# Kernel tuning notes

Hardware: AMD Instinct MI355X
Metric: run time of the kernel (lower is better)

Reference implementation:

```python
import jax, jax.numpy as jnp
import numpy as np

N = 100000
E = 1600000
IN_C = 256
HID = 128
OUT_C = 128
HEADS = 4
C_HEAD = HID // HEADS
BN_EPS = 1e-5
NEG_SLOPE = 0.2


def setup_inputs() -> dict:
    key = jax.random.key(0)
    ks = jax.random.split(key, 12)
    s = lambda fan: 1.0 / np.sqrt(fan)
    return {
        "x": jax.random.normal(ks[0], (N, IN_C), dtype=jnp.float32),
        "W_gat": jax.random.normal(ks[1], (IN_C, HID), dtype=jnp.float32) * s(IN_C),
        "att_src": jax.random.normal(ks[2], (HEADS, C_HEAD), dtype=jnp.float32) * s(C_HEAD),
        "att_dst": jax.random.normal(ks[3], (HEADS, C_HEAD), dtype=jnp.float32) * s(C_HEAD),
        "bias_gat": jnp.zeros((HID,), dtype=jnp.float32),
        "bn1_gamma": jnp.ones((HID,), dtype=jnp.float32),
        "bn1_beta": jnp.zeros((HID,), dtype=jnp.float32),
        "eps_gin": jnp.zeros((), dtype=jnp.float32),
        "lin_W": jax.random.normal(ks[4], (HID, OUT_C), dtype=jnp.float32) * s(HID),
        "lin_b": jnp.zeros((OUT_C,), dtype=jnp.float32),
        "bn2_gamma": jnp.ones((OUT_C,), dtype=jnp.float32),
        "bn2_beta": jnp.zeros((OUT_C,), dtype=jnp.float32),
        "edge_index": jax.random.randint(ks[5], (2, E), 0, N, dtype=jnp.int64),
    }


def batch_norm(h, gamma, beta):
    mu = jnp.mean(h, axis=0)
    var = jnp.var(h, axis=0)
    return (h - mu) * jax.lax.rsqrt(var + BN_EPS) * gamma + beta


def reference(x, W_gat, att_src, att_dst, bias_gat, bn1_gamma, bn1_beta,
              eps_gin, lin_W, lin_b, bn2_gamma, bn2_beta, edge_index):
    src, dst = edge_index[0], edge_index[1]
    # ---- GATConv ----
    h = (x @ W_gat).reshape(N, HEADS, C_HEAD)              # [N,H,C]
    a_src = jnp.einsum('nhc,hc->nh', h, att_src)            # [N,H]
    a_dst = jnp.einsum('nhc,hc->nh', h, att_dst)            # [N,H]
    e = jax.nn.leaky_relu(a_src[src] + a_dst[dst], NEG_SLOPE)  # [E,H]
    # segment softmax over incoming edges of each dst node
    m = jax.ops.segment_max(e, dst, num_segments=N)         # [N,H]
    num = jnp.exp(e - m[dst])                                # [E,H]
    den = jax.ops.segment_sum(num, dst, num_segments=N)      # [N,H]
    alpha = num / den[dst]                                   # [E,H]
    msg = alpha[:, :, None] * h[src]                         # [E,H,C]
    out1 = jax.ops.segment_sum(msg, dst, num_segments=N)     # [N,H,C]
    out1 = out1.reshape(N, HID) + bias_gat
    # BN + ELU (dropout = identity in eval)
    out1 = jax.nn.elu(batch_norm(out1, bn1_gamma, bn1_beta))
    # ---- GINConv: nn((1+eps)*x + sum_neighbors) ----
    agg = jax.ops.segment_sum(out1[src], dst, num_segments=N)
    z = (1.0 + eps_gin) * out1 + agg
    out2 = z @ lin_W + lin_b
    out2 = jax.nn.elu(batch_norm(out2, bn2_gamma, bn2_beta))
    return out2
```

## Files before the change

kernel.cpp:

```cpp
#include <hip/hip_runtime.h>

#define N_NODES 100000
#define N_EDGES 1600000
#define IN_C 256
#define HID 128
#define NEG_SLOPE 0.2f
#define BN_EPS 1e-5f
#define NBUCK 391
#define NPART 391
#define PART_E 4096
#define BPAD 5120
#define ELEM_BLOCKS 2048

typedef unsigned int uint32;
typedef __attribute__((ext_vector_type(8))) short bf16x8;
typedef __attribute__((ext_vector_type(4))) float f32x4;

__device__ __forceinline__ float lrelu(float x) { return x > 0.f ? x : NEG_SLOPE * x; }

__device__ __forceinline__ unsigned short f2bf(float f) {
    uint32 u = __float_as_uint(f);
    u += 0x7fffu + ((u >> 16) & 1u);
    return (unsigned short)(u >> 16);
}
__device__ __forceinline__ float bf2f(unsigned short h) {
    return __uint_as_float(((uint32)h) << 16);
}
__device__ __forceinline__ float bflo(uint32 v) { return __uint_as_float(v << 16); }
__device__ __forceinline__ float bfhi(uint32 v) { return __uint_as_float(v & 0xffff0000u); }
__device__ __forceinline__ uint32 packbf(float a, float b) {
    return (uint32)f2bf(a) | ((uint32)f2bf(b) << 16);
}

__global__ void k_transpose_all(const float* __restrict__ W1, const float* __restrict__ W2,
                                unsigned short* __restrict__ Wt1,
                                unsigned short* __restrict__ Wt2,
                                int* __restrict__ gcursor, float* __restrict__ bnacc,
                                int* __restrict__ row_ptr) {
    int t = threadIdx.x;
    if (blockIdx.x == 0) {
        for (int i = t; i < NBUCK + 1; i += 256) gcursor[i] = 0;
        bnacc[t] = 0.f;
        bnacc[256 + t] = 0.f;
        if (t == 0) row_ptr[N_NODES] = N_EDGES;
    }
    int idx = blockIdx.x * 256 + t;
    if (idx < IN_C * 128) {
        int k = idx >> 7, n = idx & 127;
        Wt1[n * IN_C + k] = f2bf(W1[idx]);
    } else {
        idx -= IN_C * 128;
        if (idx < HID * 128) {
            int k = idx >> 7, n = idx & 127;
            Wt2[n * HID + k] = f2bf(W2[idx]);
        }
    }
}

template <bool AF32, bool OUTF32, bool ATT, bool STATS>
__global__ __launch_bounds__(256) void k_gemm(const void* __restrict__ Av,
                                              const unsigned short* __restrict__ Wt,
                                              void* __restrict__ Out, int K,
                                              const float* __restrict__ att_s,
                                              const float* __restrict__ att_d,
                                              float* __restrict__ a_src,
                                              float* __restrict__ a_dst,
                                              float* __restrict__ bnst) {
    __shared__ unsigned short As[128 * 72];
    __shared__ unsigned short Bs[128 * 72];
    const int t = threadIdx.x;
    const int n0 = blockIdx.x * 128;
    const int wv = t >> 6, lane = t & 63;
    const int wy = wv >> 1, wx = wv & 1;
    const int lm = lane & 15, lg = lane >> 4;
    const float* Af = (const float*)Av;
    const unsigned short* Ah = (const unsigned short*)Av;

    f32x4 acc[4][4];
#pragma unroll
    for (int i = 0; i < 4; ++i)
#pragma unroll
        for (int j = 0; j < 4; ++j) acc[i][j] = (f32x4){0.f, 0.f, 0.f, 0.f};

    float4 afp[8];
    uint4 ahp[4];
    uint4 bvp[4];

    if (AF32) {
#pragma unroll
        for (int p = 0; p < 8; ++p) {
            int idx = p * 256 + t, row = idx >> 4, c4 = idx & 15, gn = n0 + row;
            afp[p] = (gn < N_NODES) ? *(const float4*)&Af[(size_t)gn * K + c4 * 4]
                                    : make_float4(0.f, 0.f, 0.f, 0.f);
        }
    } else {
#pragma unroll
        for (int p = 0; p < 4; ++p) {
            int idx = p * 256 + t, row = idx >> 3, c = idx & 7, gn = n0 + row;
            ahp[p] = (gn < N_NODES) ? *(const uint4*)&Ah[(size_t)gn * K + c * 8]
                                    : make_uint4(0, 0, 0, 0);
        }
    }
#pragma unroll
    for (int p = 0; p < 4; ++p) {
        int idx = p * 256 + t, n = idx >> 3, c = idx & 7;
        bvp[p] = *(const uint4*)&Wt[(size_t)n * K + c * 8];
    }

    for (int kc = 0; kc < K; kc += 64) {
        if (AF32) {
#pragma unroll
            for (int p = 0; p < 8; ++p) {
                int idx = p * 256 + t, row = idx >> 4, c4 = idx & 15;
                ushort4 b;
                b.x = f2bf(afp[p].x); b.y = f2bf(afp[p].y);
                b.z = f2bf(afp[p].z); b.w = f2bf(afp[p].w);
                *(ushort4*)&As[row * 72 + c4 * 4] = b;
            }
        } else {
#pragma unroll
            for (int p = 0; p < 4; ++p) {
                int idx = p * 256 + t, row = idx >> 3, c = idx & 7;
                *(uint4*)&As[row * 72 + c * 8] = ahp[p];
            }
        }
#pragma unroll
        for (int p = 0; p < 4; ++p) {
            int idx = p * 256 + t, n = idx >> 3, c = idx & 7;
            *(uint4*)&Bs[n * 72 + c * 8] = bvp[p];
        }
        __syncthreads();
        int kn = kc + 64;
        if (kn < K) {
            if (AF32) {
#pragma unroll
                for (int p = 0; p < 8; ++p) {
                    int idx = p * 256 + t, row = idx >> 4, c4 = idx & 15, gn = n0 + row;
                    afp[p] = (gn < N_NODES) ? *(const float4*)&Af[(size_t)gn * K + kn + c4 * 4]
                                            : make_float4(0.f, 0.f, 0.f, 0.f);
                }
            } else {
#pragma unroll
                for (int p = 0; p < 4; ++p) {
                    int idx = p * 256 + t, row = idx >> 3, c = idx & 7, gn = n0 + row;
                    ahp[p] = (gn < N_NODES) ? *(const uint4*)&Ah[(size_t)gn * K + kn + c * 8]
                                            : make_uint4(0, 0, 0, 0);
                }
            }
#pragma unroll
            for (int p = 0; p < 4; ++p) {
                int idx = p * 256 + t, n = idx >> 3, c = idx & 7;
                bvp[p] = *(const uint4*)&Wt[(size_t)n * K + kn + c * 8];
            }
        }
#pragma unroll
        for (int ks = 0; ks < 2; ++ks) {
            bf16x8 af[4], bfr[4];
#pragma unroll
            for (int i = 0; i < 4; ++i)
                af[i] = *(const bf16x8*)&As[(wy * 64 + i * 16 + lm) * 72 + ks * 32 + lg * 8];
#pragma unroll
            for (int j = 0; j < 4; ++j)
                bfr[j] = *(const bf16x8*)&Bs[(wx * 64 + j * 16 + lm) * 72 + ks * 32 + lg * 8];
#pragma unroll
            for (int i = 0; i < 4; ++i)
#pragma unroll
                for (int j = 0; j < 4; ++j)
                    acc[i][j] = __builtin_amdgcn_mfma_f32_16x16x32_bf16(af[i], bfr[j],
                                                                        acc[i][j], 0, 0, 0);
        }
        __syncthreads();
    }

    float as_w[4], ad_w[4];
    if (ATT) {
#pragma unroll
        for (int j = 0; j < 4; ++j) {
            int col = wx * 64 + j * 16 + lm;
            as_w[j] = att_s[col];
            ad_w[j] = att_d[col];
        }
    }
    float ls[4] = {0.f, 0.f, 0.f, 0.f}, lq[4] = {0.f, 0.f, 0.f, 0.f};
#pragma unroll
    for (int i = 0; i < 4; ++i) {
#pragma unroll
        for (int r = 0; r < 4; ++r) {
            int row = n0 + wy * 64 + i * 16 + lg * 4 + r;
            float v0 = acc[i][0][r], v1 = acc[i][1][r];
            float v2 = acc[i][2][r], v3 = acc[i][3][r];
            if (row < N_NODES) {
                if (OUTF32) {
                    float* op = (float*)Out + (size_t)row * 128 + wx * 64 + lm;
                    op[0] = v0; op[16] = v1; op[32] = v2; op[48] = v3;
                } else {
                    unsigned short* op =
                        (unsigned short*)Out + (size_t)row * 128 + wx * 64 + lm;
                    op[0] = f2bf(v0); op[16] = f2bf(v1);
                    op[32] = f2bf(v2); op[48] = f2bf(v3);
                }
            }
            if (STATS) {
                ls[0] += v0; lq[0] += v0 * v0;
                ls[1] += v1; lq[1] += v1 * v1;
                ls[2] += v2; lq[2] += v2 * v2;
                ls[3] += v3; lq[3] += v3 * v3;
            }
            if (ATT) {
                float ps0 = v0 * as_w[0] + v1 * as_w[1];
                float ps1 = v2 * as_w[2] + v3 * as_w[3];
                float pd0 = v0 * ad_w[0] + v1 * ad_w[1];
                float pd1 = v2 * ad_w[2] + v3 * ad_w[3];
#pragma unroll
                for (int m = 1; m < 16; m <<= 1) {
                    ps0 += __shfl_xor(ps0, m); ps1 += __shfl_xor(ps1, m);
                    pd0 += __shfl_xor(pd0, m); pd1 += __shfl_xor(pd1, m);
                }
                if (lm == 0 && row < N_NODES) {
                    *(float2*)&a_src[row * 4 + wx * 2] = make_float2(ps0, ps1);
                    *(float2*)&a_dst[row * 4 + wx * 2] = make_float2(pd0, pd1);
                }
            }
        }
    }
    if (STATS) {
#pragma unroll
        for (int j = 0; j < 4; ++j) {
            float s = ls[j], q = lq[j];
            s += __shfl_xor(s, 16); s += __shfl_xor(s, 32);
            q += __shfl_xor(q, 16); q += __shfl_xor(q, 32);
            if (lg == 0) {
                int col = wx * 64 + j * 16 + lm;
                atomicAdd(&bnst[col], s);
                atomicAdd(&bnst[128 + col], q);
            }
        }
    }
}

__global__ __launch_bounds__(256) void k_partition(const int* __restrict__ ei,
                                                   int* __restrict__ gcursor,
                                                   int* __restrict__ staging) {
    __shared__ int hist[NBUCK];
    __shared__ int loff[NBUCK];
    __shared__ int gbase[NBUCK];
    __shared__ int lstage[PART_E];
    __shared__ int gaddr[PART_E];
    __shared__ int scanbuf[512];
    int t = threadIdx.x;
    int e0 = blockIdx.x * PART_E;
    int cntAll = min(PART_E, N_EDGES - e0);
    for (int i = t; i < NBUCK; i += 256) hist[i] = 0;
    __syncthreads();
    int pk[16];
    short bb[16], rr[16];
#pragma unroll
    for (int u = 0; u < 16; ++u) {
        int e = e0 + u * 256 + t;
        bb[u] = -1;
        rr[u] = 0;
        if (e < N_EDGES) {
            int s = ei[e], d = ei[N_EDGES + e];
            int b = d >> 8;
            int r = atomicAdd(&hist[b], 1);
            pk[u] = ((d & 255) << 17) | s;
            bb[u] = (short)b;
            rr[u] = (short)r;
        }
    }
    __syncthreads();
    scanbuf[t] = (t < NBUCK) ? hist[t] : 0;
    scanbuf[t + 256] = (t + 256 < NBUCK) ? hist[t + 256] : 0;
    __syncthreads();
    for (int off = 1; off < 512; off <<= 1) {
        int a0 = scanbuf[t];
        int a1 = scanbuf[t + 256];
        int b0 = (t >= off) ? scanbuf[t - off] : 0;
        int b1 = (t + 256 >= off) ? scanbuf[t + 256 - off] : 0;
        __syncthreads();
        scanbuf[t] = a0 + b0;
        scanbuf[t + 256] = a1 + b1;
        __syncthreads();
    }
    for (int i = t; i < NBUCK; i += 256) {
        loff[i] = scanbuf[i] - hist[i];
        gbase[i] = hist[i] ? atomicAdd(&gcursor[i], hist[i]) : 0;
    }
    __syncthreads();
#pragma unroll
    for (int u = 0; u < 16; ++u) {
        if (bb[u] >= 0) {
            int b = bb[u], r = rr[u];
            int pos = loff[b] + r;
            lstage[pos] = pk[u];
            gaddr[pos] = b * BPAD + gbase[b] + r;
        }
    }
    __syncthreads();
    for (int i = t; i < cntAll; i += 256) staging[gaddr[i]] = lstage[i];
}

__global__ __launch_bounds__(256) void k_bucket_sort(const int* __restrict__ staging,
                                                     const int* __restrict__ cnts,
                                                     int* __restrict__ row_ptr,
                                                     int* __restrict__ sorted_src) {
    __shared__ int hist[256];
    __shared__ int sh[256];
    __shared__ int spill[256][2];
    __shared__ int spill_cnt;
    __shared__ int obs[4];
    int t = threadIdx.x, b = blockIdx.x;
    int part = 0;
    for (int i = t; i < b; i += 256) part += cnts[i];
#pragma unroll
    for (int m = 1; m < 64; m <<= 1) part += __shfl_xor(part, m);
    if ((t & 63) == 0) obs[t >> 6] = part;
    int cnt = cnts[b];
    hist[t] = 0;
    if (t == 0) spill_cnt = 0;
    __syncthreads();
    int ob = obs[0] + obs[1] + obs[2] + obs[3];
    const int* sb = staging + b * BPAD;
    int ent[18], rnk[18];
#pragma unroll
    for (int u = 0; u < 18; ++u) {
        int i = u * 256 + t;
        ent[u] = -1;
        rnk[u] = 0;
        if (i < cnt) {
            int p = sb[i];
            ent[u] = p;
            rnk[u] = atomicAdd(&hist[p >> 17], 1);
        }
    }
    for (int i = 18 * 256 + t; i < cnt; i += 256) {
        int p = sb[i];
        int r = atomicAdd(&hist[p >> 17], 1);
        int si = atomicAdd(&spill_cnt, 1);
        spill[si][0] = p;
        spill[si][1] = r;
    }
    __syncthreads();
    int v0 = hist[t];
    int val = v0;
    sh[t] = val;
    __syncthreads();
    for (int off = 1; off < 256; off <<= 1) {
        int o = (t >= off) ? sh[t - off] : 0;
        __syncthreads();
        val += o;
        sh[t] = val;
        __syncthreads();
    }
    int excl = val - v0;
    int d = b * 256 + t;
    if (d < N_NODES) row_ptr[d] = ob + excl;
    __syncthreads();
    hist[t] = excl;
    __syncthreads();
#pragma unroll
    for (int u = 0; u < 18; ++u) {
        if (ent[u] >= 0) {
            int p = ent[u];
            sorted_src[ob + hist[p >> 17] + rnk[u]] = p & 0x1FFFF;
        }
    }
    for (int i = t; i < spill_cnt; i += 256) {
        int p = spill[i][0];
        sorted_src[ob + hist[p >> 17] + spill[i][1]] = p & 0x1FFFF;
    }
}

__global__ __launch_bounds__(256) void k_gat_agg(const uint32* __restrict__ h32,
                                                 const float* __restrict__ a_src,
                                                 const float* __restrict__ a_dst,
                                                 const int* __restrict__ row_ptr,
                                                 const int* __restrict__ sorted_src,
                                                 uint32* __restrict__ out1) {
    __shared__ alignas(16) float wbuf[4][4][72];
    int lane = threadIdx.x & 63, wv = threadIdx.x >> 6;
    int hd = lane >> 4;
    int node = blockIdx.x * 4 + wv;
    int start = row_ptr[node];
    int deg = row_ptr[node + 1] - start;
    if (deg == 0) {
        out1[((uint32)node << 6) + lane] = 0u;
        return;
    }
    float4 ad = *(const float4*)&a_dst[node * 4];
    float acc0 = 0.f, acc1 = 0.f, den = 0.f;
    for (int j0 = 0; j0 < deg; j0 += 64) {
        int m = min(64, deg - j0);
        int s = 0;
        float4 w = make_float4(0.f, 0.f, 0.f, 0.f);
        if (lane < m) {
            s = sorted_src[start + j0 + lane];
            float4 as = *(const float4*)&a_src[s * 4];
            w.x = __expf(lrelu(as.x + ad.x));
            w.y = __expf(lrelu(as.y + ad.y));
            w.z = __expf(lrelu(as.z + ad.z));
            w.w = __expf(lrelu(as.w + ad.w));
        }
        wbuf[wv][0][lane] = w.x;
        wbuf[wv][1][lane] = w.y;
        wbuf[wv][2][lane] = w.z;
        wbuf[wv][3][lane] = w.w;
        __builtin_amdgcn_wave_barrier();
        int e0 = 0;
        for (; e0 + 8 <= m; e0 += 8) {
            uint32 hr[8];
#pragma unroll
            for (int k = 0; k < 8; ++k) {
                int ss = __builtin_amdgcn_readlane(s, e0 + k);
                hr[k] = h32[((uint32)ss << 6) + lane];
            }
            float4 w0 = *(const float4*)&wbuf[wv][hd][e0];
            float4 w1 = *(const float4*)&wbuf[wv][hd][e0 + 4];
            float wk[8] = {w0.x, w0.y, w0.z, w0.w, w1.x, w1.y, w1.z, w1.w};
#pragma unroll
            for (int k = 0; k < 8; ++k) {
                den += wk[k];
                acc0 = fmaf(wk[k], bflo(hr[k]), acc0);
                acc1 = fmaf(wk[k], bfhi(hr[k]), acc1);
            }
        }
        for (; e0 < m; ++e0) {
            int ss = __builtin_amdgcn_readlane(s, e0);
            uint32 hv = h32[((uint32)ss << 6) + lane];
            float wk = wbuf[wv][hd][e0];
            den += wk;
            acc0 = fmaf(wk, bflo(hv), acc0);
            acc1 = fmaf(wk, bfhi(hv), acc1);
        }
        __builtin_amdgcn_wave_barrier();
    }
    float rden = 1.f / den;
    out1[((uint32)node << 6) + lane] = packbf(acc0 * rden, acc1 * rden);
}

__global__ __launch_bounds__(256) void k_gin_agg(const uint32* __restrict__ ob,
                                                 const int* __restrict__ row_ptr,
                                                 const int* __restrict__ sorted_src,
                                                 const float* __restrict__ eps_ptr,
                                                 const float* __restrict__ acc_,
                                                 const float* __restrict__ gamma,
                                                 const float* __restrict__ beta,
                                                 uint32* __restrict__ zb) {
    int lane = threadIdx.x & 63, wv = threadIdx.x >> 6;
    int c0 = lane * 2;
    float mu0 = acc_[c0] * (1.f / N_NODES), mu1 = acc_[c0 + 1] * (1.f / N_NODES);
    float va0 = acc_[128 + c0] * (1.f / N_NODES) - mu0 * mu0;
    float va1 = acc_[128 + c0 + 1] * (1.f / N_NODES) - mu1 * mu1;
    float s0 = rsqrtf(va0 + BN_EPS) * gamma[c0];
    float s1 = rsqrtf(va1 + BN_EPS) * gamma[c0 + 1];
    float h0 = beta[c0] - mu0 * s0;
    float h1 = beta[c0 + 1] - mu1 * s1;
    int node = blockIdx.x * 4 + wv;
    int start = row_ptr[node];
    int deg = row_ptr[node + 1] - start;
    float acc0 = 0.f, acc1 = 0.f;
    for (int j0 = 0; j0 < deg; j0 += 64) {
        int m = min(64, deg - j0);
        int s = 0;
        if (lane < m) s = sorted_src[start + j0 + lane];
        int e0 = 0;
        for (; e0 + 8 <= m; e0 += 8) {
            uint32 hr[8];
#pragma unroll
            for (int k = 0; k < 8; ++k) {
                int ss = __builtin_amdgcn_readlane(s, e0 + k);
                hr[k] = ob[((uint32)ss << 6) + lane];
            }
#pragma unroll
            for (int k = 0; k < 8; ++k) {
                float f0 = fmaf(bflo(hr[k]), s0, h0);
                float f1 = fmaf(bfhi(hr[k]), s1, h1);
                acc0 += f0 > 0.f ? f0 : __expf(f0) - 1.f;
                acc1 += f1 > 0.f ? f1 : __expf(f1) - 1.f;
            }
        }
        for (; e0 < m; ++e0) {
            int ss = __builtin_amdgcn_readlane(s, e0);
            uint32 hv = ob[((uint32)ss << 6) + lane];
            float f0 = fmaf(bflo(hv), s0, h0);
            float f1 = fmaf(bfhi(hv), s1, h1);
            acc0 += f0 > 0.f ? f0 : __expf(f0) - 1.f;
            acc1 += f1 > 0.f ? f1 : __expf(f1) - 1.f;
        }
    }
    float ep = 1.f + eps_ptr[0];
    uint32 own = ob[((uint32)node << 6) + lane];
    float f0 = fmaf(bflo(own), s0, h0);
    float f1 = fmaf(bfhi(own), s1, h1);
    f0 = f0 > 0.f ? f0 : __expf(f0) - 1.f;
    f1 = f1 > 0.f ? f1 : __expf(f1) - 1.f;
    zb[((uint32)node << 6) + lane] = packbf(fmaf(ep, f0, acc0), fmaf(ep, f1, acc1));
}

__global__ __launch_bounds__(256) void k_bnstats_bf16(const uint32* __restrict__ buf,
                                                      float* __restrict__ acc) {
    __shared__ float sh[4][64][4];
    int lane = threadIdx.x & 63, grp = threadIdx.x >> 6;
    float s0 = 0.f, s1 = 0.f, q0 = 0.f, q1 = 0.f;
    for (int r = blockIdx.x * 4 + grp; r < N_NODES; r += gridDim.x * 4) {
        uint32 v = buf[(size_t)r * 64 + lane];
        float v0 = bflo(v), v1 = bfhi(v);
        s0 += v0; s1 += v1; q0 += v0 * v0; q1 += v1 * v1;
    }
    sh[grp][lane][0] = s0; sh[grp][lane][1] = s1;
    sh[grp][lane][2] = q0; sh[grp][lane][3] = q1;
    __syncthreads();
    if (grp == 0) {
#pragma unroll
        for (int g = 1; g < 4; ++g) {
            s0 += sh[g][lane][0]; s1 += sh[g][lane][1];
            q0 += sh[g][lane][2]; q1 += sh[g][lane][3];
        }
        int c0 = lane * 2;
        atomicAdd(&acc[c0], s0);
        atomicAdd(&acc[c0 + 1], s1);
        atomicAdd(&acc[128 + c0], q0);
        atomicAdd(&acc[128 + c0 + 1], q1);
    }
}

__global__ __launch_bounds__(256) void k_bn_elu_out(const uint32* __restrict__ in,
                                                    const float* __restrict__ acc,
                                                    const float* __restrict__ gamma,
                                                    const float* __restrict__ beta,
                                                    float2* __restrict__ out) {
    int t = threadIdx.x;
    int c0 = (t & 63) * 2;
    float mu0 = acc[c0] * (1.f / N_NODES), mu1 = acc[c0 + 1] * (1.f / N_NODES);
    float va0 = acc[128 + c0] * (1.f / N_NODES) - mu0 * mu0;
    float va1 = acc[128 + c0 + 1] * (1.f / N_NODES) - mu1 * mu1;
    float s0 = rsqrtf(va0 + BN_EPS) * gamma[c0];
    float s1 = rsqrtf(va1 + BN_EPS) * gamma[c0 + 1];
    float h0 = beta[c0] - mu0 * s0;
    float h1 = beta[c0 + 1] - mu1 * s1;
    for (size_t i = (size_t)blockIdx.x * 256 + t; i < (size_t)N_NODES * 64;
         i += (size_t)ELEM_BLOCKS * 256) {
        uint32 v = in[i];
        float r0 = fmaf(bflo(v), s0, h0);
        float r1 = fmaf(bfhi(v), s1, h1);
        r0 = r0 > 0.f ? r0 : __expf(r0) - 1.f;
        r1 = r1 > 0.f ? r1 : __expf(r1) - 1.f;
        out[i] = make_float2(r0, r1);
    }
}

extern "C" void kernel_launch(void* const* d_in, const int* in_sizes, int n_in,
                              void* d_out, int out_size, void* d_ws, size_t ws_size,
                              hipStream_t stream) {
    (void)in_sizes; (void)n_in; (void)out_size; (void)ws_size;
    const float* x       = (const float*)d_in[0];
    const float* W_gat   = (const float*)d_in[1];
    const float* att_src = (const float*)d_in[2];
    const float* att_dst = (const float*)d_in[3];
    const float* bn1_g   = (const float*)d_in[5];
    const float* bn1_b   = (const float*)d_in[6];
    const float* eps_gin = (const float*)d_in[7];
    const float* lin_W   = (const float*)d_in[8];
    const float* bn2_g   = (const float*)d_in[10];
    const float* bn2_b   = (const float*)d_in[11];
    const int*   ei      = (const int*)d_in[12];
    float* out = (float*)d_out;

    char* w = (char*)d_ws;
    size_t o = 0;
    auto take = [&](size_t b) -> char* {
        char* p = w + o;
        o += (b + 255) & ~(size_t)255;
        return p;
    };
    unsigned short* hb   = (unsigned short*)take((size_t)N_NODES * 128 * 2);
    unsigned short* Wt1  = (unsigned short*)take((size_t)128 * IN_C * 2);
    unsigned short* Wt2  = (unsigned short*)take((size_t)128 * HID * 2);
    uint32* o1b          = (uint32*)take((size_t)N_NODES * 64 * 4);
    float* a_src         = (float*)take((size_t)N_NODES * 4 * 4);
    float* a_dst         = (float*)take((size_t)N_NODES * 4 * 4);
    int*   sorted        = (int*)take((size_t)N_EDGES * 4);
    int*   staging       = (int*)take((size_t)NBUCK * BPAD * 4);
    int*   row_ptr       = (int*)take((size_t)(N_NODES + 1) * 4);
    int*   gcursor       = (int*)take((NBUCK + 1) * 4);
    float* bnacc         = (float*)take(512 * 4);
    uint32* zb  = (uint32*)hb;
    uint32* o2b = o1b;
    const int nGemmBlocks = (N_NODES + 127) / 128;

    k_transpose_all<<<((IN_C + HID) * 128 + 255) / 256, 256, 0, stream>>>(
        W_gat, lin_W, Wt1, Wt2, gcursor, bnacc, row_ptr);
    k_gemm<true, false, true, false><<<nGemmBlocks, 256, 0, stream>>>(
        x, Wt1, hb, IN_C, att_src, att_dst, a_src, a_dst, nullptr);
    k_partition<<<NPART, 256, 0, stream>>>(ei, gcursor, staging);
    k_bucket_sort<<<NBUCK, 256, 0, stream>>>(staging, gcursor, row_ptr, sorted);
    k_gat_agg<<<N_NODES / 4, 256, 0, stream>>>((const uint32*)hb, a_src, a_dst, row_ptr,
                                               sorted, o1b);
    k_bnstats_bf16<<<512, 256, 0, stream>>>(o1b, bnacc);
    k_gin_agg<<<N_NODES / 4, 256, 0, stream>>>(o1b, row_ptr, sorted, eps_gin, bnacc,
                                               bn1_g, bn1_b, zb);
    k_gemm<false, false, false, true><<<nGemmBlocks, 256, 0, stream>>>(
        zb, Wt2, o2b, HID, nullptr, nullptr, nullptr, nullptr, bnacc + 256);
    k_bn_elu_out<<<ELEM_BLOCKS, 256, 0, stream>>>(o2b, bnacc + 256, bn2_g, bn2_b,
                                                  (float2*)out);
}
```

Measured before the change: 501.0 us.

## Merge independent prep stages into shared launches to overlap partition, transpose, sort, GEMM

The weight transpose now runs inside the edge-partition kernel as extra blocks, and the first GEMM runs inside the bucket-sort kernel as extra blocks, so independent work shares launches and can overlap on the GPU. The gcursor zeroing moves to a hipMemsetAsync. This removes two kernel launches and the idle tail between small kernels. In exchange, the merged kernels take the larger shared-memory footprint of their two branches, which may lower occupancy for the GEMM blocks.

New measurement: 482.7 us. -3.6%, faster.

```diff
diff --git a/kernel.cpp b/kernel.cpp
--- a/kernel.cpp
+++ b/kernel.cpp
@@ -10,6 +10,7 @@
 #define NPART 391
 #define PART_E 4096
 #define BPAD 5120
+#define TBLOCKS 192
 #define ELEM_BLOCKS 2048
 
 typedef unsigned int uint32;
@@ -32,44 +33,19 @@
     return (uint32)f2bf(a) | ((uint32)f2bf(b) << 16);
 }
 
-__global__ void k_transpose_all(const float* __restrict__ W1, const float* __restrict__ W2,
-                                unsigned short* __restrict__ Wt1,
-                                unsigned short* __restrict__ Wt2,
-                                int* __restrict__ gcursor, float* __restrict__ bnacc,
-                                int* __restrict__ row_ptr) {
-    int t = threadIdx.x;
-    if (blockIdx.x == 0) {
-        for (int i = t; i < NBUCK + 1; i += 256) gcursor[i] = 0;
-        bnacc[t] = 0.f;
-        bnacc[256 + t] = 0.f;
-        if (t == 0) row_ptr[N_NODES] = N_EDGES;
-    }
-    int idx = blockIdx.x * 256 + t;
-    if (idx < IN_C * 128) {
-        int k = idx >> 7, n = idx & 127;
-        Wt1[n * IN_C + k] = f2bf(W1[idx]);
-    } else {
-        idx -= IN_C * 128;
-        if (idx < HID * 128) {
-            int k = idx >> 7, n = idx & 127;
-            Wt2[n * HID + k] = f2bf(W2[idx]);
-        }
-    }
-}
-
 template <bool AF32, bool OUTF32, bool ATT, bool STATS>
-__global__ __launch_bounds__(256) void k_gemm(const void* __restrict__ Av,
-                                              const unsigned short* __restrict__ Wt,
-                                              void* __restrict__ Out, int K,
-                                              const float* __restrict__ att_s,
-                                              const float* __restrict__ att_d,
-                                              float* __restrict__ a_src,
-                                              float* __restrict__ a_dst,
-                                              float* __restrict__ bnst) {
+__device__ __forceinline__ void gemm_dev(int bid, const void* __restrict__ Av,
+                                         const unsigned short* __restrict__ Wt,
+                                         void* __restrict__ Out, int K,
+                                         const float* __restrict__ att_s,
+                                         const float* __restrict__ att_d,
+                                         float* __restrict__ a_src,
+                                         float* __restrict__ a_dst,
+                                         float* __restrict__ bnst) {
     __shared__ unsigned short As[128 * 72];
     __shared__ unsigned short Bs[128 * 72];
     const int t = threadIdx.x;
-    const int n0 = blockIdx.x * 128;
+    const int n0 = bid * 128;
     const int wv = t >> 6, lane = t & 63;
     const int wy = wv >> 1, wx = wv & 1;
     const int lm = lane & 15, lg = lane >> 4;
@@ -238,16 +214,113 @@
     }
 }
 
-__global__ __launch_bounds__(256) void k_partition(const int* __restrict__ ei,
-                                                   int* __restrict__ gcursor,
-                                                   int* __restrict__ staging) {
+__device__ __forceinline__ void bucket_sort_dev(int b, const int* __restrict__ staging,
+                                                const int* __restrict__ cnts,
+                                                int* __restrict__ row_ptr,
+                                                int* __restrict__ sorted_src) {
+    __shared__ int hist[256];
+    __shared__ int sh[256];
+    __shared__ int spill[256][2];
+    __shared__ int spill_cnt;
+    __shared__ int obs[4];
+    int t = threadIdx.x;
+    int part = 0;
+    for (int i = t; i < b; i += 256) part += cnts[i];
+#pragma unroll
+    for (int m = 1; m < 64; m <<= 1) part += __shfl_xor(part, m);
+    if ((t & 63) == 0) obs[t >> 6] = part;
+    int cnt = cnts[b];
+    hist[t] = 0;
+    if (t == 0) spill_cnt = 0;
+    __syncthreads();
+    int ob = obs[0] + obs[1] + obs[2] + obs[3];
+    const int* sb = staging + b * BPAD;
+    int ent[18], rnk[18];
+#pragma unroll
+    for (int u = 0; u < 18; ++u) {
+        int i = u * 256 + t;
+        ent[u] = -1;
+        rnk[u] = 0;
+        if (i < cnt) {
+            int p = sb[i];
+            ent[u] = p;
+            rnk[u] = atomicAdd(&hist[p >> 17], 1);
+        }
+    }
+    for (int i = 18 * 256 + t; i < cnt; i += 256) {
+        int p = sb[i];
+        int r = atomicAdd(&hist[p >> 17], 1);
+        int si = atomicAdd(&spill_cnt, 1);
+        spill[si][0] = p;
+        spill[si][1] = r;
+    }
+    __syncthreads();
+    int v0 = hist[t];
+    int val = v0;
+    sh[t] = val;
+    __syncthreads();
+    for (int off = 1; off < 256; off <<= 1) {
+        int o = (t >= off) ? sh[t - off] : 0;
+        __syncthreads();
+        val += o;
+        sh[t] = val;
+        __syncthreads();
+    }
+    int excl = val - v0;
+    int d = b * 256 + t;
+    if (d < N_NODES) row_ptr[d] = ob + excl;
+    __syncthreads();
+    hist[t] = excl;
+    __syncthreads();
+#pragma unroll
+    for (int u = 0; u < 18; ++u) {
+        if (ent[u] >= 0) {
+            int p = ent[u];
+            sorted_src[ob + hist[p >> 17] + rnk[u]] = p & 0x1FFFF;
+        }
+    }
+    for (int i = t; i < spill_cnt; i += 256) {
+        int p = spill[i][0];
+        sorted_src[ob + hist[p >> 17] + spill[i][1]] = p & 0x1FFFF;
+    }
+}
+
+__global__ __launch_bounds__(256) void k_prep(const int* __restrict__ ei,
+                                              int* __restrict__ gcursor,
+                                              int* __restrict__ staging,
+                                              const float* __restrict__ W1,
+                                              const float* __restrict__ W2,
+                                              unsigned short* __restrict__ Wt1,
+                                              unsigned short* __restrict__ Wt2,
+                                              float* __restrict__ bnacc,
+                                              int* __restrict__ row_ptr) {
+    int t = threadIdx.x;
+    if (blockIdx.x >= NPART) {
+        int tb = blockIdx.x - NPART;
+        if (tb == 0) {
+            bnacc[t] = 0.f;
+            bnacc[256 + t] = 0.f;
+            if (t == 0) row_ptr[N_NODES] = N_EDGES;
+        }
+        int idx = tb * 256 + t;
+        if (idx < IN_C * 128) {
+            int k = idx >> 7, n = idx & 127;
+            Wt1[n * IN_C + k] = f2bf(W1[idx]);
+        } else {
+            idx -= IN_C * 128;
+            if (idx < HID * 128) {
+                int k = idx >> 7, n = idx & 127;
+                Wt2[n * HID + k] = f2bf(W2[idx]);
+            }
+        }
+        return;
+    }
     __shared__ int hist[NBUCK];
     __shared__ int loff[NBUCK];
     __shared__ int gbase[NBUCK];
     __shared__ int lstage[PART_E];
     __shared__ int gaddr[PART_E];
     __shared__ int scanbuf[512];
-    int t = threadIdx.x;
     int e0 = blockIdx.x * PART_E;
     int cntAll = min(PART_E, N_EDGES - e0);
     for (int i = t; i < NBUCK; i += 256) hist[i] = 0;
@@ -300,75 +373,31 @@
     for (int i = t; i < cntAll; i += 256) staging[gaddr[i]] = lstage[i];
 }
 
-__global__ __launch_bounds__(256) void k_bucket_sort(const int* __restrict__ staging,
-                                                     const int* __restrict__ cnts,
-                                                     int* __restrict__ row_ptr,
-                                                     int* __restrict__ sorted_src) {
-    __shared__ int hist[256];
-    __shared__ int sh[256];
-    __shared__ int spill[256][2];
-    __shared__ int spill_cnt;
-    __shared__ int obs[4];
-    int t = threadIdx.x, b = blockIdx.x;
-    int part = 0;
-    for (int i = t; i < b; i += 256) part += cnts[i];
-#pragma unroll
-    for (int m = 1; m < 64; m <<= 1) part += __shfl_xor(part, m);
-    if ((t & 63) == 0) obs[t >> 6] = part;
-    int cnt = cnts[b];
-    hist[t] = 0;
-    if (t == 0) spill_cnt = 0;
-    __syncthreads();
-    int ob = obs[0] + obs[1] + obs[2] + obs[3];
-    const int* sb = staging + b * BPAD;
-    int ent[18], rnk[18];
-#pragma unroll
-    for (int u = 0; u < 18; ++u) {
-        int i = u * 256 + t;
-        ent[u] = -1;
-        rnk[u] = 0;
-        if (i < cnt) {
-            int p = sb[i];
-            ent[u] = p;
-            rnk[u] = atomicAdd(&hist[p >> 17], 1);
-        }
-    }
-    for (int i = 18 * 256 + t; i < cnt; i += 256) {
-        int p = sb[i];
-        int r = atomicAdd(&hist[p >> 17], 1);
-        int si = atomicAdd(&spill_cnt, 1);
-        spill[si][0] = p;
-        spill[si][1] = r;
-    }
-    __syncthreads();
-    int v0 = hist[t];
-    int val = v0;
-    sh[t] = val;
-    __syncthreads();
-    for (int off = 1; off < 256; off <<= 1) {
-        int o = (t >= off) ? sh[t - off] : 0;
-        __syncthreads();
-        val += o;
-        sh[t] = val;
-        __syncthreads();
-    }
-    int excl = val - v0;
-    int d = b * 256 + t;
-    if (d < N_NODES) row_ptr[d] = ob + excl;
-    __syncthreads();
-    hist[t] = excl;
-    __syncthreads();
-#pragma unroll
-    for (int u = 0; u < 18; ++u) {
-        if (ent[u] >= 0) {
-            int p = ent[u];
-            sorted_src[ob + hist[p >> 17] + rnk[u]] = p & 0x1FFFF;
-        }
-    }
-    for (int i = t; i < spill_cnt; i += 256) {
-        int p = spill[i][0];
-        sorted_src[ob + hist[p >> 17] + spill[i][1]] = p & 0x1FFFF;
-    }
+__global__ __launch_bounds__(256) void k_gemm1_sort(const int* __restrict__ staging,
+                                                    const int* __restrict__ cnts,
+                                                    int* __restrict__ row_ptr,
+                                                    int* __restrict__ sorted_src,
+                                                    const float* __restrict__ x,
+                                                    const unsigned short* __restrict__ Wt1,
+                                                    unsigned short* __restrict__ hb,
+                                                    const float* __restrict__ att_s,
+                                                    const float* __restrict__ att_d,
+                                                    float* __restrict__ a_src,
+                                                    float* __restrict__ a_dst) {
+    if (blockIdx.x < NBUCK) {
+        bucket_sort_dev(blockIdx.x, staging, cnts, row_ptr, sorted_src);
+    } else {
+        gemm_dev<true, false, true, false>(blockIdx.x - NBUCK, x, Wt1, hb, IN_C,
+                                           att_s, att_d, a_src, a_dst, nullptr);
+    }
+}
+
+__global__ __launch_bounds__(256) void k_gemm2(const void* __restrict__ Av,
+                                               const unsigned short* __restrict__ Wt,
+                                               void* __restrict__ Out,
+                                               float* __restrict__ bnst) {
+    gemm_dev<false, false, false, true>(blockIdx.x, Av, Wt, Out, HID,
+                                        nullptr, nullptr, nullptr, nullptr, bnst);
 }
 
 __global__ __launch_bounds__(256) void k_gat_agg(const uint32* __restrict__ h32,
@@ -588,19 +617,17 @@
     uint32* o2b = o1b;
     const int nGemmBlocks = (N_NODES + 127) / 128;
 
-    k_transpose_all<<<((IN_C + HID) * 128 + 255) / 256, 256, 0, stream>>>(
-        W_gat, lin_W, Wt1, Wt2, gcursor, bnacc, row_ptr);
-    k_gemm<true, false, true, false><<<nGemmBlocks, 256, 0, stream>>>(
-        x, Wt1, hb, IN_C, att_src, att_dst, a_src, a_dst, nullptr);
-    k_partition<<<NPART, 256, 0, stream>>>(ei, gcursor, staging);
-    k_bucket_sort<<<NBUCK, 256, 0, stream>>>(staging, gcursor, row_ptr, sorted);
+    hipMemsetAsync(gcursor, 0, (NBUCK + 1) * sizeof(int), stream);
+    k_prep<<<NPART + TBLOCKS, 256, 0, stream>>>(ei, gcursor, staging, W_gat, lin_W,
+                                                Wt1, Wt2, bnacc, row_ptr);
+    k_gemm1_sort<<<NBUCK + nGemmBlocks, 256, 0, stream>>>(
+        staging, gcursor, row_ptr, sorted, x, Wt1, hb, att_src, att_dst, a_src, a_dst);
     k_gat_agg<<<N_NODES / 4, 256, 0, stream>>>((const uint32*)hb, a_src, a_dst, row_ptr,
                                                sorted, o1b);
     k_bnstats_bf16<<<512, 256, 0, stream>>>(o1b, bnacc);
     k_gin_agg<<<N_NODES / 4, 256, 0, stream>>>(o1b, row_ptr, sorted, eps_gin, bnacc,
                                                bn1_g, bn1_b, zb);
-    k_gemm<false, false, false, true><<<nGemmBlocks, 256, 0, stream>>>(
-        zb, Wt2, o2b, HID, nullptr, nullptr, nullptr, nullptr, bnacc + 256);
+    k_gemm2<<<nGemmBlocks, 256, 0, stream>>>(zb, Wt2, o2b, bnacc + 256);
     k_bn_elu_out<<<ELEM_BLOCKS, 256, 0, stream>>>(o2b, bnacc + 256, bn2_g, bn2_b,
                                                   (float2*)out);
 }
```
